# Optimization experiments

Measured on AMD Instinct MI355X. Metric: run time of the kernel, lower is better.

The kernel has to match this reference:

```python
import jax, jax.numpy as jnp
import numpy as np

D_MODEL = 512
NUM_HEADS = 8
D_K = D_MODEL // NUM_HEADS


def setup_inputs() -> dict:
    key = jax.random.key(0)
    ks = jax.random.split(key, 9)
    B, T = 4, 2048
    s = 1.0 / np.sqrt(D_MODEL)
    inp = {"x": jax.random.normal(ks[0], (B, T, D_MODEL), dtype=jnp.float32)}
    names = ["wq", "wk", "wv", "wo"]
    for i, n in enumerate(names):
        inp[n] = jax.random.uniform(ks[1 + i], (D_MODEL, D_MODEL), dtype=jnp.float32, minval=-s, maxval=s)
        inp["b" + n[1]] = jax.random.uniform(ks[5 + i], (D_MODEL,), dtype=jnp.float32, minval=-s, maxval=s)
    return inp


def reference(x, wq, bq, wk, bk, wv, bv, wo, bo):
    B, T, C = x.shape
    # Linear projections (torch Linear: x @ W^T + b)
    q = x @ wq.T + bq
    k = x @ wk.T + bk
    v = x @ wv.T + bv
    # [B, H, T, d_k]
    q = q.reshape(B, T, NUM_HEADS, D_K).transpose(0, 2, 1, 3)
    k = k.reshape(B, T, NUM_HEADS, D_K).transpose(0, 2, 1, 3)
    v = v.reshape(B, T, NUM_HEADS, D_K).transpose(0, 2, 1, 3)
    # scaled dot-product attention, full [B,H,T,T] scores materialized (faithful)
    scores = jnp.einsum('bhqd,bhkd->bhqk', q, k) / jnp.sqrt(jnp.float32(D_K))
    weights = jax.nn.softmax(scores, axis=-1)
    attn = jnp.einsum('bhqk,bhkd->bhqd', weights, v)
    attn = attn.transpose(0, 2, 1, 3).reshape(B, T, C)
    return attn @ wo.T + bo
```

## Files before the change

### kernel.cpp

```cpp
#include <hip/hip_runtime.h>

typedef __bf16 bf16x8 __attribute__((ext_vector_type(8)));
typedef __bf16 bf16x4 __attribute__((ext_vector_type(4)));
typedef float f32x4 __attribute__((ext_vector_type(4)));
typedef float f32x16 __attribute__((ext_vector_type(16)));

#define MFMA_16x16x32(a, b, c) __builtin_amdgcn_mfma_f32_16x16x32_bf16((a), (b), (c), 0, 0, 0)
#define MFMA32(a, b, c) __builtin_amdgcn_mfma_f32_32x32x16_bf16((a), (b), (c), 0, 0, 0)

#define WAIT_LGKM0() do { \
    asm volatile("s_waitcnt lgkmcnt(0)" ::: "memory"); \
    __builtin_amdgcn_sched_barrier(0); } while (0)

typedef const __attribute__((address_space(1))) void GVp;
typedef __attribute__((address_space(3))) void LVp;
#define GLOAD16(gp, lp) \
    __builtin_amdgcn_global_load_lds((GVp*)(gp), (LVp*)(lp), 16, 0, 0)

__device__ __forceinline__ float fexp2(float x) {
    float r;
    asm("v_exp_f32 %0, %1" : "=v"(r) : "v"(x));
    return r;
}

__device__ __forceinline__ unsigned cvtpk(float lo, float hi) {
    unsigned r;
    asm("v_cvt_pk_bf16_f32 %0, %1, %2" : "=v"(r) : "v"(lo), "v"(hi));
    return r;
}
#define PSWAP(a, b) asm volatile("v_permlane32_swap_b32 %0, %1" : "+v"(a), "+v"(b))

union PB { unsigned u[4]; bf16x8 v; };

__device__ __forceinline__ int swz(int row, int colb) {
    return row * 128 + (colb ^ ((row & 7) << 4));
}

__global__ __launch_bounds__(256) void cvt_all(const float* __restrict__ x,
                                               const float* __restrict__ w0,
                                               const float* __restrict__ w1,
                                               const float* __restrict__ w2,
                                               const float* __restrict__ w3,
                                               __bf16* __restrict__ xo,
                                               __bf16* __restrict__ o0,
                                               __bf16* __restrict__ o1,
                                               __bf16* __restrict__ o2,
                                               __bf16* __restrict__ o3) {
    int i = blockIdx.x * 256 + threadIdx.x;
    const float* in;
    __bf16* out;
    int idx;
    if (i < 1048576) {
        in = x; out = xo; idx = i;
    } else {
        int j = i - 1048576;
        int s = j >> 16;
        idx = j & 65535;
        in = (s == 0) ? w0 : (s == 1) ? w1 : (s == 2) ? w2 : w3;
        out = (s == 0) ? o0 : (s == 1) ? o1 : (s == 2) ? o2 : o3;
    }
    float4 v = ((const float4*)in)[idx];
    bf16x4 o;
    o[0] = (__bf16)v.x; o[1] = (__bf16)v.y; o[2] = (__bf16)v.z; o[3] = (__bf16)v.w;
    ((bf16x4*)out)[idx] = o;
}

template <typename OT, bool VT, int BM, int BN>
__device__ __forceinline__ void gemm_body(const __bf16* __restrict__ A,
                                          const __bf16* __restrict__ Bw,
                                          const float* __restrict__ bias,
                                          OT* __restrict__ C,
                                          int K, int N, float scale) {
    const int m0 = blockIdx.x * BM;
    const int n0 = blockIdx.y * BN;
    const int tid = threadIdx.x;
    const int l = tid & 63, w = tid >> 6;
    constexpr int MI = BM / 32;
    constexpr int NI = BN / 32;
    const int wr = w >> 1, wc = w & 1;
    const int lr = l & 15;
    const int lkb = (l >> 4) << 4;

    __shared__ __bf16 As[BM * 64];
    __shared__ __bf16 Bs[BN * 64];
    char* AsC = (char*)As;
    char* BsC = (char*)Bs;

    const int srow = tid >> 3;
    const int c8 = ((tid & 7) ^ (srow & 7)) * 8;

    f32x4 acc[MI][NI] = {};

    for (int k0 = 0; k0 < K; k0 += 64) {
        __syncthreads();
#pragma unroll
        for (int p = 0; p < BM / 32; ++p)
            GLOAD16(A + (size_t)(m0 + p * 32 + srow) * K + k0 + c8,
                    AsC + p * 4096 + tid * 16);
#pragma unroll
        for (int p = 0; p < BN / 32; ++p)
            GLOAD16(Bw + (size_t)(n0 + p * 32 + srow) * K + k0 + c8,
                    BsC + p * 4096 + tid * 16);
        __syncthreads();
#pragma unroll
        for (int kk = 0; kk < 2; ++kk) {
            bf16x8 af[MI], bfr[NI];
#pragma unroll
            for (int mi = 0; mi < MI; ++mi)
                af[mi] = *(const bf16x8*)(AsC + swz(wr * (BM / 2) + mi * 16 + lr, kk * 64 + lkb));
#pragma unroll
            for (int ni = 0; ni < NI; ++ni)
                bfr[ni] = *(const bf16x8*)(BsC + swz(wc * (BN / 2) + ni * 16 + lr, kk * 64 + lkb));
#pragma unroll
            for (int mi = 0; mi < MI; ++mi)
#pragma unroll
                for (int ni = 0; ni < NI; ++ni)
                    acc[mi][ni] = MFMA_16x16x32(af[mi], bfr[ni], acc[mi][ni]);
        }
    }

    const int rb = (l >> 4) * 4;
#pragma unroll
    for (int mi = 0; mi < MI; ++mi) {
#pragma unroll
        for (int ni = 0; ni < NI; ++ni) {
            int gn = n0 + wc * (BN / 2) + ni * 16 + lr;
            int gm = m0 + wr * (BM / 2) + mi * 16 + rb;
            float bv = bias[gn];
            if constexpr (VT) {
                bf16x4 o4;
#pragma unroll
                for (int j = 0; j < 4; ++j)
                    o4[j] = (__bf16)((acc[mi][ni][j] + bv) * scale);
                *(bf16x4*)((__bf16*)C + ((size_t)(gm >> 11) << 20) +
                           (size_t)gn * 2048 + (gm & 2047)) = o4;
            } else {
#pragma unroll
                for (int j = 0; j < 4; ++j) {
                    float v = (acc[mi][ni][j] + bv) * scale;
                    C[(size_t)(gm + j) * N + gn] = (OT)v;
                }
            }
        }
    }
}

#define QSCALE 0.18033688f

__global__ __launch_bounds__(256) void qkv_gemm(const __bf16* __restrict__ X,
                                                const __bf16* __restrict__ Wq,
                                                const __bf16* __restrict__ Wk,
                                                const __bf16* __restrict__ Wv,
                                                const float* __restrict__ bq,
                                                const float* __restrict__ bk,
                                                const float* __restrict__ bv,
                                                __bf16* __restrict__ Qo,
                                                __bf16* __restrict__ Ko,
                                                __bf16* __restrict__ Vto) {
    int z = blockIdx.z;
    if (z == 0) {
        gemm_body<__bf16, false, 64, 128>(X, Wq, bq, Qo, 512, 512, QSCALE);
    } else if (z == 1) {
        gemm_body<__bf16, false, 64, 128>(X, Wk, bk, Ko, 512, 512, 1.0f);
    } else {
        gemm_body<__bf16, true, 64, 128>(X, Wv, bv, Vto, 512, 512, 1.0f);
    }
}

__global__ __launch_bounds__(256) void out_gemm_fused(const __bf16* __restrict__ Op0,
                                                      const __bf16* __restrict__ Op1,
                                                      const float* __restrict__ lsum,
                                                      const __bf16* __restrict__ W,
                                                      const float* __restrict__ bias,
                                                      float* __restrict__ C) {
    const int m0 = blockIdx.x * 64;
    const int n0 = blockIdx.y * 128;
    const int tid = threadIdx.x;
    const int l = tid & 63, w = tid >> 6;
    const int wr = w >> 1, wc = w & 1;
    const int lr = l & 15;
    const int lkb = (l >> 4) << 4;

    __shared__ __bf16 As[64 * 64];
    __shared__ __bf16 Bs[128 * 64];
    __shared__ float2 wts[8][64];
    char* AsC = (char*)As;
    char* BsC = (char*)Bs;

    const int b = m0 >> 11, q0 = m0 & 2047;

#pragma unroll
    for (int j = 0; j < 2; ++j) {
        int idx = tid + j * 256;
        int i = idx & 63, hh = idx >> 6;
        size_t r = (size_t)(b * 8 + hh) * 2048 + q0 + i;
        float l0v = lsum[r], l1v = lsum[65536 + r];
        float inv = 1.f / (l0v + l1v);
        wts[hh][i] = make_float2(l0v * inv, l1v * inv);
    }

    const int srow = tid >> 3;
    const int c8 = ((tid & 7) ^ (srow & 7)) * 8;

    f32x4 acc[2][4] = {};

    for (int k0 = 0; k0 < 512; k0 += 64) {
        __syncthreads();
        const int hh = k0 >> 6;
#pragma unroll
        for (int p = 0; p < 2; ++p) {
            int row = p * 32 + srow;
            size_t r = (size_t)(b * 8 + hh) * 2048 + q0 + row;
            float2 wt = wts[hh][row];
            bf16x8 o0 = *(const bf16x8*)(Op0 + r * 64 + c8);
            bf16x8 o1 = *(const bf16x8*)(Op1 + r * 64 + c8);
            bf16x8 mg;
#pragma unroll
            for (int jj = 0; jj < 8; ++jj)
                mg[jj] = (__bf16)((float)o0[jj] * wt.x + (float)o1[jj] * wt.y);
            *(bf16x8*)(AsC + p * 4096 + tid * 16) = mg;
        }
#pragma unroll
        for (int p = 0; p < 4; ++p)
            GLOAD16(W + (size_t)(n0 + p * 32 + srow) * 512 + k0 + c8,
                    BsC + p * 4096 + tid * 16);
        __syncthreads();
#pragma unroll
        for (int kk = 0; kk < 2; ++kk) {
            bf16x8 af[2], bfr[4];
#pragma unroll
            for (int mi = 0; mi < 2; ++mi)
                af[mi] = *(const bf16x8*)(AsC + swz(wr * 32 + mi * 16 + lr, kk * 64 + lkb));
#pragma unroll
            for (int ni = 0; ni < 4; ++ni)
                bfr[ni] = *(const bf16x8*)(BsC + swz(wc * 64 + ni * 16 + lr, kk * 64 + lkb));
#pragma unroll
            for (int mi = 0; mi < 2; ++mi)
#pragma unroll
                for (int ni = 0; ni < 4; ++ni)
                    acc[mi][ni] = MFMA_16x16x32(af[mi], bfr[ni], acc[mi][ni]);
        }
    }

    const int rb = (l >> 4) * 4;
#pragma unroll
    for (int mi = 0; mi < 2; ++mi) {
#pragma unroll
        for (int ni = 0; ni < 4; ++ni) {
            int gn = n0 + wc * 64 + ni * 16 + lr;
            int gm = m0 + wr * 32 + mi * 16 + rb;
            float bv = bias[gn];
#pragma unroll
            for (int j = 0; j < 4; ++j)
                C[(size_t)(gm + j) * 512 + gn] = acc[mi][ni][j] + bv;
        }
    }
}

__global__ __launch_bounds__(256, 2) void attn_fwd(const __bf16* __restrict__ Q,
                                                   const __bf16* __restrict__ K,
                                                   const __bf16* __restrict__ Vt,
                                                   __bf16* __restrict__ Op0,
                                                   __bf16* __restrict__ Op1,
                                                   float* __restrict__ lsum) {
    const int T = 2048, Cm = 512;
    const int qt0 = blockIdx.x * 128;
    const int h = blockIdx.y;
    const int half = blockIdx.z & 1, b = blockIdx.z >> 1;
    const int kt0 = half * 1024, kend = kt0 + 1024;
    const int tid = threadIdx.x;
    const int l = tid & 63, w = tid >> 6;
    const int q5 = l & 31, hi = l >> 5;
    const size_t rbase = ((size_t)b * T) * Cm + h * 64;
    const size_t vtbase = ((size_t)b << 20) + (size_t)(h * 64) * 2048;

    __shared__ __align__(16) char smem[33280];

    const int grow = tid >> 3;
    const int gcol = ((tid & 7) ^ (grow & 7)) * 8;
    const __bf16* kgp = K + rbase + (size_t)grow * Cm + gcol;
    const __bf16* vgp = Vt + vtbase + (size_t)grow * 2048 + gcol;

#define ATTN_STAGE(nb, ktv)                                                   \
    do {                                                                      \
        char* kd_ = smem + (nb) * 8192 + tid * 16;                            \
        char* vd_ = smem + 16384 + (nb) * 8192 + tid * 16;                    \
        _Pragma("unroll")                                                     \
        for (int p = 0; p < 2; ++p) {                                         \
            GLOAD16(kgp + (size_t)((ktv) + p * 32) * Cm, kd_ + p * 4096);     \
            GLOAD16(vgp + (size_t)(p * 32) * 2048 + (ktv), vd_ + p * 4096);   \
        }                                                                     \
    } while (0)

    bf16x8 qf[4];
#pragma unroll
    for (int dc = 0; dc < 4; ++dc)
        qf[dc] = *(const bf16x8*)(Q + rbase +
            (size_t)(qt0 + w * 32 + q5) * Cm + dc * 16 + hi * 8);

    f32x16 oa[2] = {};
    float l_r = 0.f;

    ATTN_STAGE(0, kt0);
    __syncthreads();

    char* albase = smem + 32768 + w * 128;

    int cur = 0;
    for (int kt = kt0; kt < kend; kt += 64, cur ^= 1) {
        if (kt + 64 < kend) ATTN_STAGE(cur ^ 1, kt + 64);

        const char* kb_ = smem + cur * 8192;
        f32x16 s0 = {}, s1 = {};
#pragma unroll
        for (int dc = 0; dc < 4; ++dc) {
            bf16x8 kf0 = *(const bf16x8*)(kb_ + swz(q5, dc * 32 + hi * 16));
            bf16x8 kf1 = *(const bf16x8*)(kb_ + swz(32 + q5, dc * 32 + hi * 16));
            __builtin_amdgcn_s_setprio(1);
            s0 = MFMA32(kf0, qf[dc], s0);
            s1 = MFMA32(kf1, qf[dc], s1);
            __builtin_amdgcn_s_setprio(0);
        }

        float rs = 0.f;
#pragma unroll
        for (int r = 0; r < 16; ++r) {
            float p0 = fexp2(s0[r]);
            float p1 = fexp2(s1[r]);
            s0[r] = p0; s1[r] = p1;
            rs += p0 + p1;
        }
        rs += __shfl_xor(rs, 32);
        l_r += rs;

        PB pf[4];
#pragma unroll
        for (int kb = 0; kb < 2; ++kb) {
#pragma unroll
            for (int cc = 0; cc < 2; ++cc) {
                int gA = 8 * cc, gB = 8 * cc + 4;
                float a0, a1, a2, a3, b0, b1, b2, b3;
                if (kb == 0) {
                    a0 = s0[gA]; a1 = s0[gA + 1]; a2 = s0[gA + 2]; a3 = s0[gA + 3];
                    b0 = s0[gB]; b1 = s0[gB + 1]; b2 = s0[gB + 2]; b3 = s0[gB + 3];
                } else {
                    a0 = s1[gA]; a1 = s1[gA + 1]; a2 = s1[gA + 2]; a3 = s1[gA + 3];
                    b0 = s1[gB]; b1 = s1[gB + 1]; b2 = s1[gB + 2]; b3 = s1[gB + 3];
                }
                unsigned w0A = cvtpk(a0, a1), w1A = cvtpk(a2, a3);
                unsigned w0B = cvtpk(b0, b1), w1B = cvtpk(b2, b3);
                PSWAP(w0A, w0B);
                PSWAP(w1A, w1B);
                int kc = 2 * kb + cc;
                pf[kc].u[0] = w0A; pf[kc].u[1] = w1A;
                pf[kc].u[2] = w0B; pf[kc].u[3] = w1B;
            }
        }

        const char* vb_ = smem + 16384 + cur * 8192;
#pragma unroll
        for (int kc = 0; kc < 4; ++kc) {
            bf16x8 vf0 = *(const bf16x8*)(vb_ + swz(q5, kc * 32 + hi * 16));
            bf16x8 vf1 = *(const bf16x8*)(vb_ + swz(32 + q5, kc * 32 + hi * 16));
            __builtin_amdgcn_s_setprio(1);
            oa[0] = MFMA32(pf[kc].v, vf0, oa[0]);
            oa[1] = MFMA32(pf[kc].v, vf1, oa[1]);
            __builtin_amdgcn_s_setprio(0);
        }

        __syncthreads();
    }

    {
        float invl = 1.f / l_r;
        *(float*)(albase + q5 * 4) = invl;
        WAIT_LGKM0();
        f32x4 ivr[4];
#pragma unroll
        for (int rg = 0; rg < 4; ++rg)
            ivr[rg] = *(const f32x4*)(albase + hi * 16 + rg * 32);
        __bf16* Opb = half ? Op1 : Op0;
        const size_t rr = (size_t)(b * 8 + h) * 2048;
#pragma unroll
        for (int rg = 0; rg < 4; ++rg)
#pragma unroll
            for (int c = 0; c < 4; ++c) {
                int qr = qt0 + w * 32 + 8 * rg + 4 * hi + c;
                float iv = ivr[rg][c];
                Opb[(rr + qr) * 64 + q5]      = (__bf16)(oa[0][4 * rg + c] * iv);
                Opb[(rr + qr) * 64 + 32 + q5] = (__bf16)(oa[1][4 * rg + c] * iv);
            }
        if (hi == 0)
            lsum[(size_t)half * 65536 + rr + qt0 + w * 32 + q5] = l_r;
    }
#undef ATTN_STAGE
}

extern "C" void kernel_launch(void* const* d_in, const int* in_sizes, int n_in,
                              void* d_out, int out_size, void* d_ws, size_t ws_size,
                              hipStream_t stream) {
    const float* x  = (const float*)d_in[0];
    const float* wq = (const float*)d_in[1];
    const float* bq = (const float*)d_in[2];
    const float* wk = (const float*)d_in[3];
    const float* bk = (const float*)d_in[4];
    const float* wv = (const float*)d_in[5];
    const float* bv = (const float*)d_in[6];
    const float* wo = (const float*)d_in[7];
    const float* bo = (const float*)d_in[8];

    char* ws = (char*)d_ws;
    __bf16* xb    = (__bf16*)(ws);
    __bf16* Op0   = (__bf16*)(ws);
    __bf16* Qb    = (__bf16*)(ws + ((size_t)8 << 20));
    __bf16* Kb    = (__bf16*)(ws + ((size_t)16 << 20));
    __bf16* Vtb   = (__bf16*)(ws + ((size_t)24 << 20));
    __bf16* Op1   = (__bf16*)(ws + ((size_t)32 << 20));
    __bf16* wqb   = (__bf16*)(ws + ((size_t)40 << 20));
    __bf16* wkb   = (__bf16*)(ws + ((size_t)40 << 20) + ((size_t)512 << 10));
    __bf16* wvb   = (__bf16*)(ws + ((size_t)40 << 20) + ((size_t)1024 << 10));
    __bf16* wob   = (__bf16*)(ws + ((size_t)40 << 20) + ((size_t)1536 << 10));
    float*  lsb   = (float*)(ws + ((size_t)42 << 20));

    cvt_all<<<dim3(5120), dim3(256), 0, stream>>>(x, wq, wk, wv, wo,
                                                  xb, wqb, wkb, wvb, wob);
    qkv_gemm<<<dim3(128, 4, 3), dim3(256), 0, stream>>>(xb, wqb, wkb, wvb,
                                                        bq, bk, bv, Qb, Kb, Vtb);
    attn_fwd<<<dim3(16, 8, 8), dim3(256), 0, stream>>>(Qb, Kb, Vtb, Op0, Op1, lsb);
    out_gemm_fused<<<dim3(128, 4), dim3(256), 0, stream>>>(Op0, Op1, lsb, wob, bo,
                                                           (float*)d_out);
}
```

Baseline: 91.80 us.

## Process two 32-row query tiles per wave in attention to reuse K/V fragments

Each wave now handles 64 query rows (two 32-row sub-tiles) instead of 32, so each block covers 256 queries and the grid halves. K fragments are loaded from LDS once per tile and reused for both sub-tiles, and V fragments are shared across both P·V MFMA chains, cutting LDS reads and global K/V staging per query. The cost is roughly doubled accumulator and fragment registers, which may pressure occupancy under launch_bounds(256,2), and half as many blocks (512) to spread across CUs.

```diff
diff --git a/kernel.cpp b/kernel.cpp
--- a/kernel.cpp
+++ b/kernel.cpp
@@ -264,7 +264,7 @@
                                                    __bf16* __restrict__ Op1,
                                                    float* __restrict__ lsum) {
     const int T = 2048, Cm = 512;
-    const int qt0 = blockIdx.x * 128;
+    const int qt0 = blockIdx.x * 256;
     const int h = blockIdx.y;
     const int half = blockIdx.z & 1, b = blockIdx.z >> 1;
     const int kt0 = half * 1024, kend = kt0 + 1024;
@@ -274,7 +274,7 @@
     const size_t rbase = ((size_t)b * T) * Cm + h * 64;
     const size_t vtbase = ((size_t)b << 20) + (size_t)(h * 64) * 2048;
 
-    __shared__ __align__(16) char smem[33280];
+    __shared__ __align__(16) char smem[33792];
 
     const int grow = tid >> 3;
     const int gcol = ((tid & 7) ^ (grow & 7)) * 8;
@@ -292,68 +292,119 @@
         }                                                                     \
     } while (0)
 
-    bf16x8 qf[4];
-#pragma unroll
-    for (int dc = 0; dc < 4; ++dc)
-        qf[dc] = *(const bf16x8*)(Q + rbase +
-            (size_t)(qt0 + w * 32 + q5) * Cm + dc * 16 + hi * 8);
-
-    f32x16 oa[2] = {};
-    float l_r = 0.f;
+    bf16x8 qfA[4], qfB[4];
+#pragma unroll
+    for (int dc = 0; dc < 4; ++dc) {
+        qfA[dc] = *(const bf16x8*)(Q + rbase +
+            (size_t)(qt0 + w * 64 + q5) * Cm + dc * 16 + hi * 8);
+        qfB[dc] = *(const bf16x8*)(Q + rbase +
+            (size_t)(qt0 + w * 64 + 32 + q5) * Cm + dc * 16 + hi * 8);
+    }
+
+    f32x16 oaA[2] = {}, oaB[2] = {};
+    float lA = 0.f, lB = 0.f;
 
     ATTN_STAGE(0, kt0);
     __syncthreads();
 
-    char* albase = smem + 32768 + w * 128;
+    char* albase = smem + 32768 + w * 256;
 
     int cur = 0;
     for (int kt = kt0; kt < kend; kt += 64, cur ^= 1) {
         if (kt + 64 < kend) ATTN_STAGE(cur ^ 1, kt + 64);
 
         const char* kb_ = smem + cur * 8192;
-        f32x16 s0 = {}, s1 = {};
+        bf16x8 kf0[4], kf1[4];
 #pragma unroll
         for (int dc = 0; dc < 4; ++dc) {
-            bf16x8 kf0 = *(const bf16x8*)(kb_ + swz(q5, dc * 32 + hi * 16));
-            bf16x8 kf1 = *(const bf16x8*)(kb_ + swz(32 + q5, dc * 32 + hi * 16));
-            __builtin_amdgcn_s_setprio(1);
-            s0 = MFMA32(kf0, qf[dc], s0);
-            s1 = MFMA32(kf1, qf[dc], s1);
-            __builtin_amdgcn_s_setprio(0);
-        }
-
-        float rs = 0.f;
-#pragma unroll
-        for (int r = 0; r < 16; ++r) {
-            float p0 = fexp2(s0[r]);
-            float p1 = fexp2(s1[r]);
-            s0[r] = p0; s1[r] = p1;
-            rs += p0 + p1;
-        }
-        rs += __shfl_xor(rs, 32);
-        l_r += rs;
-
-        PB pf[4];
-#pragma unroll
-        for (int kb = 0; kb < 2; ++kb) {
-#pragma unroll
-            for (int cc = 0; cc < 2; ++cc) {
-                int gA = 8 * cc, gB = 8 * cc + 4;
-                float a0, a1, a2, a3, b0, b1, b2, b3;
-                if (kb == 0) {
-                    a0 = s0[gA]; a1 = s0[gA + 1]; a2 = s0[gA + 2]; a3 = s0[gA + 3];
-                    b0 = s0[gB]; b1 = s0[gB + 1]; b2 = s0[gB + 2]; b3 = s0[gB + 3];
-                } else {
-                    a0 = s1[gA]; a1 = s1[gA + 1]; a2 = s1[gA + 2]; a3 = s1[gA + 3];
-                    b0 = s1[gB]; b1 = s1[gB + 1]; b2 = s1[gB + 2]; b3 = s1[gB + 3];
+            kf0[dc] = *(const bf16x8*)(kb_ + swz(q5, dc * 32 + hi * 16));
+            kf1[dc] = *(const bf16x8*)(kb_ + swz(32 + q5, dc * 32 + hi * 16));
+        }
+
+        PB pfA[4], pfB[4];
+        {
+            f32x16 s0 = {}, s1 = {};
+#pragma unroll
+            for (int dc = 0; dc < 4; ++dc) {
+                __builtin_amdgcn_s_setprio(1);
+                s0 = MFMA32(kf0[dc], qfA[dc], s0);
+                s1 = MFMA32(kf1[dc], qfA[dc], s1);
+                __builtin_amdgcn_s_setprio(0);
+            }
+            float rs = 0.f;
+#pragma unroll
+            for (int r = 0; r < 16; ++r) {
+                float p0 = fexp2(s0[r]);
+                float p1 = fexp2(s1[r]);
+                s0[r] = p0; s1[r] = p1;
+                rs += p0 + p1;
+            }
+            rs += __shfl_xor(rs, 32);
+            lA += rs;
+#pragma unroll
+            for (int kb = 0; kb < 2; ++kb) {
+#pragma unroll
+                for (int cc = 0; cc < 2; ++cc) {
+                    int gA = 8 * cc, gB = 8 * cc + 4;
+                    float a0, a1, a2, a3, b0, b1, b2, b3;
+                    if (kb == 0) {
+                        a0 = s0[gA]; a1 = s0[gA + 1]; a2 = s0[gA + 2]; a3 = s0[gA + 3];
+                        b0 = s0[gB]; b1 = s0[gB + 1]; b2 = s0[gB + 2]; b3 = s0[gB + 3];
+                    } else {
+                        a0 = s1[gA]; a1 = s1[gA + 1]; a2 = s1[gA + 2]; a3 = s1[gA + 3];
+                        b0 = s1[gB]; b1 = s1[gB + 1]; b2 = s1[gB + 2]; b3 = s1[gB + 3];
+                    }
+                    unsigned w0A = cvtpk(a0, a1), w1A = cvtpk(a2, a3);
+                    unsigned w0B = cvtpk(b0, b1), w1B = cvtpk(b2, b3);
+                    PSWAP(w0A, w0B);
+                    PSWAP(w1A, w1B);
+                    int kc = 2 * kb + cc;
+                    pfA[kc].u[0] = w0A; pfA[kc].u[1] = w1A;
+                    pfA[kc].u[2] = w0B; pfA[kc].u[3] = w1B;
                 }
-                unsigned w0A = cvtpk(a0, a1), w1A = cvtpk(a2, a3);
-                unsigned w0B = cvtpk(b0, b1), w1B = cvtpk(b2, b3);
-                PSWAP(w0A, w0B);
-                PSWAP(w1A, w1B);
-                int kc = 2 * kb + cc;
-                pf[kc].u[0] = w0A; pf[kc].u[1] = w1A;
-                pf[kc].u[2] = w0B; pf[kc].u[3] = w1B;
+            }
+        }
+
+        {
+            f32x16 s0 = {}, s1 = {};
+#pragma unroll
+            for (int dc = 0; dc < 4; ++dc) {
+                __builtin_amdgcn_s_setprio(1);
+                s0 = MFMA32(kf0[dc], qfB[dc], s0);
+                s1 = MFMA32(kf1[dc], qfB[dc], s1);
+                __builtin_amdgcn_s_setprio(0);
+            }
+            float rs = 0.f;
+#pragma unroll
+            for (int r = 0; r < 16; ++r) {
+                float p0 = fexp2(s0[r]);
+                float p1 = fexp2(s1[r]);
+                s0[r] = p0; s1[r] = p1;
+                rs += p0 + p1;
+            }
+            rs += __shfl_xor(rs, 32);
+            lB += rs;
+#pragma unroll
+            for (int kb = 0; kb < 2; ++kb) {
+#pragma unroll
+                for (int cc = 0; cc < 2; ++cc) {
+                    int gA = 8 * cc, gB = 8 * cc + 4;
+                    float a0, a1, a2, a3, b0, b1, b2, b3;
+                    if (kb == 0) {
+                        a0 = s0[gA]; a1 = s0[gA + 1]; a2 = s0[gA + 2]; a3 = s0[gA + 3];
+                        b0 = s0[gB]; b1 = s0[gB + 1]; b2 = s0[gB + 2]; b3 = s0[gB + 3];
+                    } else {
+                        a0 = s1[gA]; a1 = s1[gA + 1]; a2 = s1[gA + 2]; a3 = s1[gA + 3];
+                        b0 = s1[gB]; b1 = s1[gB + 1]; b2 = s1[gB + 2]; b3 = s1[gB + 3];
+                    }
+                    unsigned w0A = cvtpk(a0, a1), w1A = cvtpk(a2, a3);
+                    unsigned w0B = cvtpk(b0, b1), w1B = cvtpk(b2, b3);
+                    PSWAP(w0A, w0B);
+                    PSWAP(w1A, w1B);
+                    int kc = 2 * kb + cc;
+                    pfB[kc].u[0] = w0A; pfB[kc].u[1] = w1A;
+                    pfB[kc].u[2] = w0B; pfB[kc].u[3] = w1B;
+                }
             }
         }
 
@@ -363,35 +414,57 @@
             bf16x8 vf0 = *(const bf16x8*)(vb_ + swz(q5, kc * 32 + hi * 16));
             bf16x8 vf1 = *(const bf16x8*)(vb_ + swz(32 + q5, kc * 32 + hi * 16));
             __builtin_amdgcn_s_setprio(1);
-            oa[0] = MFMA32(pf[kc].v, vf0, oa[0]);
-            oa[1] = MFMA32(pf[kc].v, vf1, oa[1]);
+            oaA[0] = MFMA32(pfA[kc].v, vf0, oaA[0]);
+            oaA[1] = MFMA32(pfA[kc].v, vf1, oaA[1]);
+            oaB[0] = MFMA32(pfB[kc].v, vf0, oaB[0]);
+            oaB[1] = MFMA32(pfB[kc].v, vf1, oaB[1]);
             __builtin_amdgcn_s_setprio(0);
         }
 
         __syncthreads();
     }
 
+    __bf16* Opb = half ? Op1 : Op0;
+    const size_t rr = (size_t)(b * 8 + h) * 2048;
     {
-        float invl = 1.f / l_r;
+        float invl = 1.f / lA;
         *(float*)(albase + q5 * 4) = invl;
         WAIT_LGKM0();
         f32x4 ivr[4];
 #pragma unroll
         for (int rg = 0; rg < 4; ++rg)
             ivr[rg] = *(const f32x4*)(albase + hi * 16 + rg * 32);
-        __bf16* Opb = half ? Op1 : Op0;
-        const size_t rr = (size_t)(b * 8 + h) * 2048;
 #pragma unroll
         for (int rg = 0; rg < 4; ++rg)
 #pragma unroll
             for (int c = 0; c < 4; ++c) {
-                int qr = qt0 + w * 32 + 8 * rg + 4 * hi + c;
+                int qr = qt0 + w * 64 + 8 * rg + 4 * hi + c;
                 float iv = ivr[rg][c];
-                Opb[(rr + qr) * 64 + q5]      = (__bf16)(oa[0][4 * rg + c] * iv);
-                Opb[(rr + qr) * 64 + 32 + q5] = (__bf16)(oa[1][4 * rg + c] * iv);
-            }
-        if (hi == 0)
-            lsum[(size_t)half * 65536 + rr + qt0 + w * 32 + q5] = l_r;
+                Opb[(rr + qr) * 64 + q5]      = (__bf16)(oaA[0][4 * rg + c] * iv);
+                Opb[(rr + qr) * 64 + 32 + q5] = (__bf16)(oaA[1][4 * rg + c] * iv);
+            }
+    }
+    {
+        float invl = 1.f / lB;
+        *(float*)(albase + 128 + q5 * 4) = invl;
+        WAIT_LGKM0();
+        f32x4 ivr[4];
+#pragma unroll
+        for (int rg = 0; rg < 4; ++rg)
+            ivr[rg] = *(const f32x4*)(albase + 128 + hi * 16 + rg * 32);
+#pragma unroll
+        for (int rg = 0; rg < 4; ++rg)
+#pragma unroll
+            for (int c = 0; c < 4; ++c) {
+                int qr = qt0 + w * 64 + 32 + 8 * rg + 4 * hi + c;
+                float iv = ivr[rg][c];
+                Opb[(rr + qr) * 64 + q5]      = (__bf16)(oaB[0][4 * rg + c] * iv);
+                Opb[(rr + qr) * 64 + 32 + q5] = (__bf16)(oaB[1][4 * rg + c] * iv);
+            }
+    }
+    if (hi == 0) {
+        lsum[(size_t)half * 65536 + rr + qt0 + w * 64 + q5] = lA;
+        lsum[(size_t)half * 65536 + rr + qt0 + w * 64 + 32 + q5] = lB;
     }
 #undef ATTN_STAGE
 }
@@ -426,7 +499,7 @@
                                                   xb, wqb, wkb, wvb, wob);
     qkv_gemm<<<dim3(128, 4, 3), dim3(256), 0, stream>>>(xb, wqb, wkb, wvb,
                                                         bq, bk, bv, Qb, Kb, Vtb);
-    attn_fwd<<<dim3(16, 8, 8), dim3(256), 0, stream>>>(Qb, Kb, Vtb, Op0, Op1, lsb);
+    attn_fwd<<<dim3(8, 8, 8), dim3(256), 0, stream>>>(Qb, Kb, Vtb, Op0, Op1, lsb);
     out_gemm_fused<<<dim3(128, 4), dim3(256), 0, stream>>>(Op0, Op1, lsb, wob, bo,
                                                            (float*)d_out);
 }
```

Result: faster. 87.45 us (-4.7%).
